# Kernel tuning notes

Hardware: AMD Instinct MI355X
Metric: run time of the kernel (lower is better)

Reference implementation:

```python
import jax, jax.numpy as jnp
import numpy as np

EMBED_DIM = 1024
NUM_HEADS = 16
HEAD_DIM = EMBED_DIM // NUM_HEADS


def setup_inputs() -> dict:
    key = jax.random.key(0)
    ks = jax.random.split(key, 5)
    x = jax.random.normal(ks[0], (2, 2048, EMBED_DIM), dtype=jnp.float32)
    s_in = 1.0 / np.sqrt(EMBED_DIM)
    W_qkv = jax.random.uniform(ks[1], (EMBED_DIM, 3 * EMBED_DIM), minval=-s_in, maxval=s_in, dtype=jnp.float32)
    b_qkv = jax.random.uniform(ks[2], (3 * EMBED_DIM,), minval=-s_in, maxval=s_in, dtype=jnp.float32)
    W_out = jax.random.uniform(ks[3], (EMBED_DIM, EMBED_DIM), minval=-s_in, maxval=s_in, dtype=jnp.float32)
    b_out = jax.random.uniform(ks[4], (EMBED_DIM,), minval=-s_in, maxval=s_in, dtype=jnp.float32)
    return {"x": x, "W_qkv": W_qkv, "b_qkv": b_qkv, "W_out": W_out, "b_out": b_out}


def reference(x, W_qkv, b_qkv, W_out, b_out):
    B, S, D = x.shape
    H, Dh = NUM_HEADS, HEAD_DIM
    qkv = x @ W_qkv + b_qkv                       # [B, S, 3D]
    q, k, v = jnp.split(qkv, 3, axis=-1)
    # [B, S, D] -> [B, H, S, Dh]
    q = q.reshape(B, S, H, Dh).transpose(0, 2, 1, 3)
    k = k.reshape(B, S, H, Dh).transpose(0, 2, 1, 3)
    v = v.reshape(B, S, H, Dh).transpose(0, 2, 1, 3)
    scores = jnp.einsum('bhqd,bhkd->bhqk', q, k) / jnp.sqrt(jnp.float32(Dh))
    probs = jax.nn.softmax(scores, axis=-1)       # [B, H, S, S]
    attn = jnp.einsum('bhqk,bhkd->bhqd', probs, v)
    attn = attn.transpose(0, 2, 1, 3).reshape(B, S, D)
    return attn @ W_out + b_out
```

## Files before the change

kernel.cpp:

```cpp
#include <hip/hip_runtime.h>
#include <hip/hip_bf16.h>

#define DEV __device__ __forceinline__

typedef __bf16 bf16x8 __attribute__((ext_vector_type(8)));
typedef float f32x4 __attribute__((ext_vector_type(4)));
typedef float f32x16 __attribute__((ext_vector_type(16)));
using u16 = unsigned short;
using u32 = unsigned int;

static constexpr int S = 2048;
static constexpr int D = 1024;
static constexpr float SCQ = 0.125f * 1.44269504088896340736f;

DEV u16 f2bf(float f) {
  unsigned u = __builtin_bit_cast(unsigned, f);
  u += 0x7fffu + ((u >> 16) & 1u);
  return (u16)(u >> 16);
}
DEV u16 f2bfr(float f) {
  return (u16)((__builtin_bit_cast(u32, f) + 0x8000u) >> 16);
}
DEV u32 pk2(float a, float b) {
  u32 ua = __builtin_bit_cast(u32, a) + 0x8000u;
  u32 ub = __builtin_bit_cast(u32, b) + 0x8000u;
  return __builtin_amdgcn_perm(ub, ua, 0x07060302);
}

DEV void gl16(const u16* __restrict__ g, u16* l) {
  __builtin_amdgcn_global_load_lds((const __attribute__((address_space(1))) u32*)g,
                                   (__attribute__((address_space(3))) u32*)l, 16, 0, 0);
}

__global__ __launch_bounds__(256) void k_prep(const float* __restrict__ x, u16* __restrict__ Xb,
                                              const float* __restrict__ Wqkv, u16* __restrict__ WqkvT,
                                              const float* __restrict__ Wout, u16* __restrict__ WoutT) {
  __shared__ float t[32][33];
  const int bid = blockIdx.x;
  const int tid = threadIdx.x;
  if (bid < 4096) {
    const int i = bid * 256 + tid;
    const float4 v = reinterpret_cast<const float4*>(x)[i];
    ushort4 o;
    o.x = f2bf(v.x); o.y = f2bf(v.y); o.z = f2bf(v.z); o.w = f2bf(v.w);
    reinterpret_cast<ushort4*>(Xb)[i] = o;
    return;
  }
  const float* in;
  u16* out;
  int R, C, bx, by;
  if (bid < 4096 + 3072) {
    const int b = bid - 4096;
    in = Wqkv; out = WqkvT; R = 1024; C = 3072;
    bx = b % 96; by = b / 96;
  } else {
    const int b = bid - 7168;
    in = Wout; out = WoutT; R = 1024; C = 1024;
    bx = b & 31; by = b >> 5;
  }
  const int tx = tid & 31, ty = tid >> 5;
  const int c0 = bx * 32, r0 = by * 32;
  for (int i = ty; i < 32; i += 8)
    t[i][tx] = in[(size_t)(r0 + i) * C + c0 + tx];
  __syncthreads();
  for (int i = ty; i < 32; i += 8)
    out[(size_t)(c0 + i) * R + r0 + tx] = f2bf(t[tx][i]);
}

template <int MODE, int TN>
__global__ __launch_bounds__(256) void k_gemm(const u16* __restrict__ A, const u16* __restrict__ Bt,
                                              const float* __restrict__ bias, int M, int N, int K,
                                              u16* __restrict__ Qb, u16* __restrict__ Kb,
                                              u16* __restrict__ Vt, float* __restrict__ outF) {
  constexpr int NJ = TN / 32;
  __shared__ u16 As[2][128][32];
  __shared__ u16 Bs[2][TN][32];
  const int tid = threadIdx.x;
  const int lane = tid & 63, wave = tid >> 6;
  const int l15 = lane & 15, quad = lane >> 4;
  const int m0 = blockIdx.y * 128, n0 = blockIdx.x * TN;
  const int wm = (wave >> 1) * 64, wn = (wave & 1) * (TN / 2);
  const int lr = lane >> 2;
  const int lcs = ((((lane & 3) - (lane >> 3)) & 3)) * 8;
  const int sq = ((quad + (l15 >> 1)) & 3) * 8;

  f32x4 acc[4][NJ];
#pragma unroll
  for (int i = 0; i < 4; i++)
#pragma unroll
    for (int j = 0; j < NJ; j++) acc[i][j] = (f32x4){0.f, 0.f, 0.f, 0.f};

  const u16* Aw0 = &A[(size_t)(m0 + wave * 32 + lr) * K + lcs];
  const u16* Aw1 = &A[(size_t)(m0 + wave * 32 + 16 + lr) * K + lcs];
  const u16* Bw0;
  const u16* Bw1;
  if constexpr (TN == 128) {
    Bw0 = &Bt[(size_t)(n0 + wave * 32 + lr) * K + lcs];
    Bw1 = &Bt[(size_t)(n0 + wave * 32 + 16 + lr) * K + lcs];
  } else {
    Bw0 = &Bt[(size_t)(n0 + wave * 16 + lr) * K + lcs];
  }

  gl16(Aw0, &As[0][wave * 32][0]);
  gl16(Aw1, &As[0][wave * 32 + 16][0]);
  if constexpr (TN == 128) {
    gl16(Bw0, &Bs[0][wave * 32][0]);
    gl16(Bw1, &Bs[0][wave * 32 + 16][0]);
  } else {
    gl16(Bw0, &Bs[0][wave * 16][0]);
  }

  int cur = 0;
#pragma unroll 2
  for (int kk = 0; kk < K; kk += 32, cur ^= 1) {
    __syncthreads();
    if (kk + 32 < K) {
      gl16(Aw0 + kk + 32, &As[cur ^ 1][wave * 32][0]);
      gl16(Aw1 + kk + 32, &As[cur ^ 1][wave * 32 + 16][0]);
      if constexpr (TN == 128) {
        gl16(Bw0 + kk + 32, &Bs[cur ^ 1][wave * 32][0]);
        gl16(Bw1 + kk + 32, &Bs[cur ^ 1][wave * 32 + 16][0]);
      } else {
        gl16(Bw0 + kk + 32, &Bs[cur ^ 1][wave * 16][0]);
      }
    }
    bf16x8 af[4], bfv[NJ];
#pragma unroll
    for (int i = 0; i < 4; i++)
      af[i] = *reinterpret_cast<const bf16x8*>(&As[cur][wm + i * 16 + l15][sq]);
#pragma unroll
    for (int j = 0; j < NJ; j++)
      bfv[j] = *reinterpret_cast<const bf16x8*>(&Bs[cur][wn + j * 16 + l15][sq]);
#pragma unroll
    for (int i = 0; i < 4; i++)
#pragma unroll
      for (int j = 0; j < NJ; j++)
        acc[i][j] = __builtin_amdgcn_mfma_f32_16x16x32_bf16(af[i], bfv[j], acc[i][j], 0, 0, 0);
  }

  if constexpr (MODE == 0) {
    __shared__ u16 LT[64][136];
    if (n0 >= 2048) {
      const int b = m0 >> 11, sbase = m0 & 2047;
#pragma unroll
      for (int p = 0; p < 2; p++) {
        __syncthreads();
        if ((wave & 1) == p) {
#pragma unroll
          for (int j = 0; j < NJ; j++) {
            const int n = n0 + wn + j * 16 + l15;
            const float vb = bias[n];
#pragma unroll
            for (int i = 0; i < 4; i++) {
              uint2 pw;
              pw.x = pk2(acc[i][j][0] + vb, acc[i][j][1] + vb);
              pw.y = pk2(acc[i][j][2] + vb, acc[i][j][3] + vb);
              *reinterpret_cast<uint2*>(&LT[j * 16 + l15][wm + i * 16 + quad * 4]) = pw;
            }
          }
        }
        __syncthreads();
        const int h = ((n0 - 2048) >> 6) + p;
        const int bh = b * 16 + h;
        const int nl = tid >> 2, cc = (tid & 3) * 32;
        u16* dst = &Vt[((size_t)bh * 64 + nl) * S + sbase + cc];
#pragma unroll
        for (int k = 0; k < 4; k++)
          reinterpret_cast<uint4*>(dst)[k] = *reinterpret_cast<const uint4*>(&LT[nl][cc + k * 8]);
      }
    } else {
#pragma unroll
      for (int i = 0; i < 4; i++) {
#pragma unroll
        for (int j = 0; j < NJ; j++) {
#pragma unroll
          for (int r = 0; r < 4; r++) {
            const int m = m0 + wm + i * 16 + quad * 4 + r;
            const int n = n0 + wn + j * 16 + l15;
            const float v = acc[i][j][r] + bias[n];
            const int h = (n >> 6) & 15, dh = n & 63;
            const int b = m >> 11, s = m & 2047;
            const int bh = b * 16 + h;
            if (n < 1024) Qb[((size_t)bh * S + s) * 64 + dh] = f2bfr(v * SCQ);
            else          Kb[((size_t)bh * S + s) * 64 + dh] = f2bfr(v);
          }
        }
      }
    }
  } else {
#pragma unroll
    for (int i = 0; i < 4; i++)
#pragma unroll
      for (int j = 0; j < NJ; j++)
#pragma unroll
        for (int r = 0; r < 4; r++) {
          const int m = m0 + wm + i * 16 + quad * 4 + r;
          const int n = n0 + wn + j * 16 + l15;
          outF[(size_t)m * N + n] = acc[i][j][r] + bias[n];
        }
  }
}

__global__ __launch_bounds__(256, 2) void k_attn(const u16* __restrict__ Qb,
                                                 const u16* __restrict__ Kb,
                                                 const u16* __restrict__ Vt,
                                                 u16* __restrict__ attnB) {
  __shared__ u16 Ks[64][72];
  __shared__ u16 Vs[64][72];
  __shared__ u16 Pl[4][32][72];
  const int bh = blockIdx.y;
  const int q0 = blockIdx.x * 128;
  const int tid = threadIdx.x;
  const int lane = tid & 63, wave = tid >> 6;
  const int l31 = lane & 31, hi = lane >> 5;
  const u16* Qh = Qb + (size_t)bh * S * 64;
  const u16* Kh = Kb + (size_t)bh * S * 64;
  const u16* Vh = Vt + (size_t)bh * 64 * S;
  const int qrow = q0 + wave * 32 + l31;
  bf16x8 qf[4];
#pragma unroll
  for (int f = 0; f < 4; f++)
    qf[f] = *reinterpret_cast<const bf16x8*>(&Qh[(size_t)qrow * 64 + f * 16 + hi * 8]);

  const int r0 = tid >> 3, c0 = (tid & 7) * 8;

  float li = 0.f;
  f32x16 o0, o1;
#pragma unroll
  for (int r = 0; r < 16; r++) { o0[r] = 0.f; o1[r] = 0.f; }

  uint4 pk0 = *reinterpret_cast<const uint4*>(&Kh[(size_t)r0 * 64 + c0]);
  uint4 pk1 = *reinterpret_cast<const uint4*>(&Kh[(size_t)(r0 + 32) * 64 + c0]);
  uint4 pv0 = *reinterpret_cast<const uint4*>(&Vh[(size_t)r0 * S + c0]);
  uint4 pv1 = *reinterpret_cast<const uint4*>(&Vh[(size_t)(r0 + 32) * S + c0]);

  for (int kb = 0; kb < S / 64; kb++) {
    __syncthreads();
    *reinterpret_cast<uint4*>(&Ks[r0][c0]) = pk0;
    *reinterpret_cast<uint4*>(&Ks[r0 + 32][c0]) = pk1;
    *reinterpret_cast<uint4*>(&Vs[r0][c0]) = pv0;
    *reinterpret_cast<uint4*>(&Vs[r0 + 32][c0]) = pv1;
    __syncthreads();
    if (kb + 1 < S / 64) {
      const u16* Kn = Kh + (size_t)(kb + 1) * 64 * 64;
      pk0 = *reinterpret_cast<const uint4*>(&Kn[(size_t)r0 * 64 + c0]);
      pk1 = *reinterpret_cast<const uint4*>(&Kn[(size_t)(r0 + 32) * 64 + c0]);
      pv0 = *reinterpret_cast<const uint4*>(&Vh[(size_t)r0 * S + (kb + 1) * 64 + c0]);
      pv1 = *reinterpret_cast<const uint4*>(&Vh[(size_t)(r0 + 32) * S + (kb + 1) * 64 + c0]);
    }
    f32x16 z[2];
#pragma unroll
    for (int kt = 0; kt < 2; kt++) {
#pragma unroll
      for (int r = 0; r < 16; r++) z[kt][r] = 0.f;
#pragma unroll
      for (int f = 0; f < 4; f++) {
        const bf16x8 a = *reinterpret_cast<const bf16x8*>(&Ks[kt * 32 + l31][f * 16 + hi * 8]);
        z[kt] = __builtin_amdgcn_mfma_f32_32x32x16_bf16(a, qf[f], z[kt], 0, 0, 0);
      }
    }
    float s0 = 0.f, s1 = 0.f, s2 = 0.f, s3 = 0.f;
#pragma unroll
    for (int kt = 0; kt < 2; kt++)
#pragma unroll
      for (int r = 0; r < 16; r++) {
        const float p = __builtin_amdgcn_exp2f(z[kt][r]);
        z[kt][r] = p;
        if ((r & 3) == 0) s0 += p; else if ((r & 3) == 1) s1 += p;
        else if ((r & 3) == 2) s2 += p; else s3 += p;
      }
    li += (s0 + s1) + (s2 + s3);
#pragma unroll
    for (int kt = 0; kt < 2; kt++)
#pragma unroll
      for (int g = 0; g < 4; g++) {
        uint2 pw;
        pw.x = pk2(z[kt][g * 4 + 0], z[kt][g * 4 + 1]);
        pw.y = pk2(z[kt][g * 4 + 2], z[kt][g * 4 + 3]);
        *reinterpret_cast<uint2*>(&Pl[wave][l31][kt * 32 + g * 8 + hi * 4]) = pw;
      }
#pragma unroll
    for (int f = 0; f < 4; f++) {
      const bf16x8 bp = *reinterpret_cast<const bf16x8*>(&Pl[wave][l31][f * 16 + hi * 8]);
      const bf16x8 av0 = *reinterpret_cast<const bf16x8*>(&Vs[l31][f * 16 + hi * 8]);
      const bf16x8 av1 = *reinterpret_cast<const bf16x8*>(&Vs[32 + l31][f * 16 + hi * 8]);
      o0 = __builtin_amdgcn_mfma_f32_32x32x16_bf16(av0, bp, o0, 0, 0, 0);
      o1 = __builtin_amdgcn_mfma_f32_32x32x16_bf16(av1, bp, o1, 0, 0, 0);
    }
  }
  li += __shfl_xor(li, 32);
  const float inv = 1.f / li;
#pragma unroll
  for (int dt = 0; dt < 2; dt++) {
    const f32x16& od = dt ? o1 : o0;
#pragma unroll
    for (int g = 0; g < 4; g++) {
      uint2 ow;
      ow.x = pk2(od[g * 4 + 0] * inv, od[g * 4 + 1] * inv);
      ow.y = pk2(od[g * 4 + 2] * inv, od[g * 4 + 3] * inv);
      *reinterpret_cast<uint2*>(&Pl[wave][l31][dt * 32 + g * 8 + hi * 4]) = ow;
    }
  }
  const int b = bh >> 4, h = bh & 15;
  const int mbase = b * S + q0 + wave * 32;
  const int qr = lane >> 1, ch = (lane & 1) * 32;
  u16* dst = &attnB[(size_t)(mbase + qr) * D + h * 64 + ch];
#pragma unroll
  for (int c = 0; c < 4; c++)
    reinterpret_cast<uint4*>(dst)[c] = *reinterpret_cast<const uint4*>(&Pl[wave][qr][ch + c * 8]);
}

extern "C" void kernel_launch(void* const* d_in, const int* in_sizes, int n_in,
                              void* d_out, int out_size, void* d_ws, size_t ws_size,
                              hipStream_t stream) {
  const float* x = (const float*)d_in[0];
  const float* Wqkv = (const float*)d_in[1];
  const float* bqkv = (const float*)d_in[2];
  const float* Wout = (const float*)d_in[3];
  const float* bout = (const float*)d_in[4];
  float* out = (float*)d_out;

  char* p = (char*)d_ws;
  u16* Xb = (u16*)p;    p += (size_t)4096 * 1024 * 2;
  u16* WqkvT = (u16*)p; p += (size_t)3072 * 1024 * 2;
  u16* WoutT = (u16*)p; p += (size_t)1024 * 1024 * 2;
  u16* Qb = (u16*)p;    p += (size_t)32 * 2048 * 64 * 2;
  u16* Kb = (u16*)p;    p += (size_t)32 * 2048 * 64 * 2;
  u16* Vt = (u16*)p;    p += (size_t)32 * 64 * 2048 * 2;
  u16* attnB = (u16*)p; p += (size_t)4096 * 1024 * 2;

  k_prep<<<4096 + 3072 + 1024, 256, 0, stream>>>(x, Xb, Wqkv, WqkvT, Wout, WoutT);
  k_gemm<0, 128><<<dim3(3072 / 128, 4096 / 128), 256, 0, stream>>>(
      Xb, WqkvT, bqkv, 4096, 3072, 1024, Qb, Kb, Vt, nullptr);
  k_attn<<<dim3(2048 / 128, 32), 256, 0, stream>>>(Qb, Kb, Vt, attnB);
  k_gemm<1, 64><<<dim3(1024 / 64, 4096 / 128), 256, 0, stream>>>(
      attnB, WoutT, bout, 4096, 1024, 1024, nullptr, nullptr, nullptr, out);
}
```

Before: 202.5 us.

## Split GEMM template; alias epilogue LDS and deepen K-tile for output projection

The templated GEMM becomes two specialized kernels. The QKV GEMM reuses the operand LDS buffers for the V-transpose staging tile and raises its occupancy hint to 5 blocks per CU. The output-projection GEMM uses a 64-wide K tile with an XOR-swizzled LDS layout, compile-time K/N and two MFMA k-steps per barrier. This halves the number of barrier iterations and reduces LDS footprint, at the cost of more registers and possible spills under the tighter launch bound.

```diff
diff --git a/kernel.cpp b/kernel.cpp
--- a/kernel.cpp
+++ b/kernel.cpp
@@ -67,14 +67,16 @@
     out[(size_t)(c0 + i) * R + r0 + tx] = f2bf(t[tx][i]);
 }
 
-template <int MODE, int TN>
-__global__ __launch_bounds__(256) void k_gemm(const u16* __restrict__ A, const u16* __restrict__ Bt,
-                                              const float* __restrict__ bias, int M, int N, int K,
-                                              u16* __restrict__ Qb, u16* __restrict__ Kb,
-                                              u16* __restrict__ Vt, float* __restrict__ outF) {
-  constexpr int NJ = TN / 32;
-  __shared__ u16 As[2][128][32];
-  __shared__ u16 Bs[2][TN][32];
+__global__ __launch_bounds__(256, 5) void k_gemm0(const u16* __restrict__ A, const u16* __restrict__ Bt,
+                                                  const float* __restrict__ bias, int M, int N, int K,
+                                                  u16* __restrict__ Qb, u16* __restrict__ Kb,
+                                                  u16* __restrict__ Vt) {
+  constexpr int TN = 128, NJ = 4;
+  constexpr int ASZ = 2 * 128 * 32 * 2;
+  __shared__ __align__(16) char smem[ASZ + 2 * TN * 32 * 2];
+  auto As = reinterpret_cast<u16(*)[128][32]>(smem);
+  auto Bs = reinterpret_cast<u16(*)[TN][32]>(smem + ASZ);
+  auto LT = reinterpret_cast<u16(*)[136]>(smem);
   const int tid = threadIdx.x;
   const int lane = tid & 63, wave = tid >> 6;
   const int l15 = lane & 15, quad = lane >> 4;
@@ -92,23 +94,13 @@
 
   const u16* Aw0 = &A[(size_t)(m0 + wave * 32 + lr) * K + lcs];
   const u16* Aw1 = &A[(size_t)(m0 + wave * 32 + 16 + lr) * K + lcs];
-  const u16* Bw0;
-  const u16* Bw1;
-  if constexpr (TN == 128) {
-    Bw0 = &Bt[(size_t)(n0 + wave * 32 + lr) * K + lcs];
-    Bw1 = &Bt[(size_t)(n0 + wave * 32 + 16 + lr) * K + lcs];
-  } else {
-    Bw0 = &Bt[(size_t)(n0 + wave * 16 + lr) * K + lcs];
-  }
+  const u16* Bw0 = &Bt[(size_t)(n0 + wave * 32 + lr) * K + lcs];
+  const u16* Bw1 = &Bt[(size_t)(n0 + wave * 32 + 16 + lr) * K + lcs];
 
   gl16(Aw0, &As[0][wave * 32][0]);
   gl16(Aw1, &As[0][wave * 32 + 16][0]);
-  if constexpr (TN == 128) {
-    gl16(Bw0, &Bs[0][wave * 32][0]);
-    gl16(Bw1, &Bs[0][wave * 32 + 16][0]);
-  } else {
-    gl16(Bw0, &Bs[0][wave * 16][0]);
-  }
+  gl16(Bw0, &Bs[0][wave * 32][0]);
+  gl16(Bw1, &Bs[0][wave * 32 + 16][0]);
 
   int cur = 0;
 #pragma unroll 2
@@ -117,12 +109,8 @@
     if (kk + 32 < K) {
       gl16(Aw0 + kk + 32, &As[cur ^ 1][wave * 32][0]);
       gl16(Aw1 + kk + 32, &As[cur ^ 1][wave * 32 + 16][0]);
-      if constexpr (TN == 128) {
-        gl16(Bw0 + kk + 32, &Bs[cur ^ 1][wave * 32][0]);
-        gl16(Bw1 + kk + 32, &Bs[cur ^ 1][wave * 32 + 16][0]);
-      } else {
-        gl16(Bw0 + kk + 32, &Bs[cur ^ 1][wave * 16][0]);
-      }
+      gl16(Bw0 + kk + 32, &Bs[cur ^ 1][wave * 32][0]);
+      gl16(Bw1 + kk + 32, &Bs[cur ^ 1][wave * 32 + 16][0]);
     }
     bf16x8 af[4], bfv[NJ];
 #pragma unroll
@@ -138,67 +126,128 @@
         acc[i][j] = __builtin_amdgcn_mfma_f32_16x16x32_bf16(af[i], bfv[j], acc[i][j], 0, 0, 0);
   }
 
-  if constexpr (MODE == 0) {
-    __shared__ u16 LT[64][136];
-    if (n0 >= 2048) {
-      const int b = m0 >> 11, sbase = m0 & 2047;
-#pragma unroll
-      for (int p = 0; p < 2; p++) {
-        __syncthreads();
-        if ((wave & 1) == p) {
-#pragma unroll
-          for (int j = 0; j < NJ; j++) {
-            const int n = n0 + wn + j * 16 + l15;
-            const float vb = bias[n];
-#pragma unroll
-            for (int i = 0; i < 4; i++) {
-              uint2 pw;
-              pw.x = pk2(acc[i][j][0] + vb, acc[i][j][1] + vb);
-              pw.y = pk2(acc[i][j][2] + vb, acc[i][j][3] + vb);
-              *reinterpret_cast<uint2*>(&LT[j * 16 + l15][wm + i * 16 + quad * 4]) = pw;
-            }
+  if (n0 >= 2048) {
+    const int b = m0 >> 11, sbase = m0 & 2047;
+#pragma unroll
+    for (int p = 0; p < 2; p++) {
+      __syncthreads();
+      if ((wave & 1) == p) {
+#pragma unroll
+        for (int j = 0; j < NJ; j++) {
+          const int n = n0 + wn + j * 16 + l15;
+          const float vb = bias[n];
+#pragma unroll
+          for (int i = 0; i < 4; i++) {
+            uint2 pw;
+            pw.x = pk2(acc[i][j][0] + vb, acc[i][j][1] + vb);
+            pw.y = pk2(acc[i][j][2] + vb, acc[i][j][3] + vb);
+            *reinterpret_cast<uint2*>(&LT[j * 16 + l15][wm + i * 16 + quad * 4]) = pw;
           }
         }
-        __syncthreads();
-        const int h = ((n0 - 2048) >> 6) + p;
-        const int bh = b * 16 + h;
-        const int nl = tid >> 2, cc = (tid & 3) * 32;
-        u16* dst = &Vt[((size_t)bh * 64 + nl) * S + sbase + cc];
-#pragma unroll
-        for (int k = 0; k < 4; k++)
-          reinterpret_cast<uint4*>(dst)[k] = *reinterpret_cast<const uint4*>(&LT[nl][cc + k * 8]);
-      }
-    } else {
-#pragma unroll
-      for (int i = 0; i < 4; i++) {
-#pragma unroll
-        for (int j = 0; j < NJ; j++) {
-#pragma unroll
-          for (int r = 0; r < 4; r++) {
-            const int m = m0 + wm + i * 16 + quad * 4 + r;
-            const int n = n0 + wn + j * 16 + l15;
-            const float v = acc[i][j][r] + bias[n];
-            const int h = (n >> 6) & 15, dh = n & 63;
-            const int b = m >> 11, s = m & 2047;
-            const int bh = b * 16 + h;
-            if (n < 1024) Qb[((size_t)bh * S + s) * 64 + dh] = f2bfr(v * SCQ);
-            else          Kb[((size_t)bh * S + s) * 64 + dh] = f2bfr(v);
-          }
-        }
-      }
+      }
+      __syncthreads();
+      const int h = ((n0 - 2048) >> 6) + p;
+      const int bh = b * 16 + h;
+      const int nl = tid >> 2, cc = (tid & 3) * 32;
+      u16* dst = &Vt[((size_t)bh * 64 + nl) * S + sbase + cc];
+#pragma unroll
+      for (int k = 0; k < 4; k++)
+        reinterpret_cast<uint4*>(dst)[k] = *reinterpret_cast<const uint4*>(&LT[nl][cc + k * 8]);
     }
   } else {
 #pragma unroll
-    for (int i = 0; i < 4; i++)
-#pragma unroll
-      for (int j = 0; j < NJ; j++)
+    for (int i = 0; i < 4; i++) {
+#pragma unroll
+      for (int j = 0; j < NJ; j++) {
 #pragma unroll
         for (int r = 0; r < 4; r++) {
           const int m = m0 + wm + i * 16 + quad * 4 + r;
           const int n = n0 + wn + j * 16 + l15;
-          outF[(size_t)m * N + n] = acc[i][j][r] + bias[n];
+          const float v = acc[i][j][r] + bias[n];
+          const int h = (n >> 6) & 15, dh = n & 63;
+          const int b = m >> 11, s = m & 2047;
+          const int bh = b * 16 + h;
+          if (n < 1024) Qb[((size_t)bh * S + s) * 64 + dh] = f2bfr(v * SCQ);
+          else          Kb[((size_t)bh * S + s) * 64 + dh] = f2bfr(v);
         }
-  }
+      }
+    }
+  }
+}
+
+__global__ __launch_bounds__(256, 2) void k_gemm2(const u16* __restrict__ A, const u16* __restrict__ Bt,
+                                                  const float* __restrict__ bias, float* __restrict__ outF) {
+  constexpr int K = 1024, N = 1024;
+  constexpr int ASZ = 2 * 128 * 64 * 2;
+  __shared__ __align__(16) char smem[ASZ + 2 * 64 * 64 * 2];
+  auto As = reinterpret_cast<u16(*)[128][64]>(smem);
+  auto Bs = reinterpret_cast<u16(*)[64][64]>(smem + ASZ);
+  const int tid = threadIdx.x;
+  const int lane = tid & 63, wave = tid >> 6;
+  const int l15 = lane & 15, quad = lane >> 4;
+  const int m0 = blockIdx.y * 128, n0 = blockIdx.x * 64;
+  const int wm = (wave >> 1) * 64, wn = (wave & 1) * 32;
+  const int srow = lane >> 3;
+  const int scol = ((lane & 7) ^ (lane >> 3)) * 8;
+
+  f32x4 acc[4][2];
+#pragma unroll
+  for (int i = 0; i < 4; i++)
+#pragma unroll
+    for (int j = 0; j < 2; j++) acc[i][j] = (f32x4){0.f, 0.f, 0.f, 0.f};
+
+  const u16* Ap[4];
+  const u16* Bp[2];
+#pragma unroll
+  for (int c = 0; c < 4; c++)
+    Ap[c] = &A[(size_t)(m0 + (wave * 4 + c) * 8 + srow) * K + scol];
+#pragma unroll
+  for (int c = 0; c < 2; c++)
+    Bp[c] = &Bt[(size_t)(n0 + (wave * 2 + c) * 8 + srow) * K + scol];
+
+#pragma unroll
+  for (int c = 0; c < 4; c++) gl16(Ap[c], &As[0][(wave * 4 + c) * 8][0]);
+#pragma unroll
+  for (int c = 0; c < 2; c++) gl16(Bp[c], &Bs[0][(wave * 2 + c) * 8][0]);
+
+  int cur = 0;
+#pragma unroll 2
+  for (int kk = 0; kk < K; kk += 64, cur ^= 1) {
+    __syncthreads();
+    if (kk + 64 < K) {
+#pragma unroll
+      for (int c = 0; c < 4; c++) gl16(Ap[c] + kk + 64, &As[cur ^ 1][(wave * 4 + c) * 8][0]);
+#pragma unroll
+      for (int c = 0; c < 2; c++) gl16(Bp[c] + kk + 64, &Bs[cur ^ 1][(wave * 2 + c) * 8][0]);
+    }
+#pragma unroll
+    for (int ks = 0; ks < 2; ks++) {
+      const int sc = ((ks * 4 + quad) ^ (l15 & 7)) * 8;
+      bf16x8 af[4], bfv[2];
+#pragma unroll
+      for (int i = 0; i < 4; i++)
+        af[i] = *reinterpret_cast<const bf16x8*>(&As[cur][wm + i * 16 + l15][sc]);
+#pragma unroll
+      for (int j = 0; j < 2; j++)
+        bfv[j] = *reinterpret_cast<const bf16x8*>(&Bs[cur][wn + j * 16 + l15][sc]);
+#pragma unroll
+      for (int i = 0; i < 4; i++)
+#pragma unroll
+        for (int j = 0; j < 2; j++)
+          acc[i][j] = __builtin_amdgcn_mfma_f32_16x16x32_bf16(af[i], bfv[j], acc[i][j], 0, 0, 0);
+    }
+  }
+
+#pragma unroll
+  for (int i = 0; i < 4; i++)
+#pragma unroll
+    for (int j = 0; j < 2; j++)
+#pragma unroll
+      for (int r = 0; r < 4; r++) {
+        const int m = m0 + wm + i * 16 + quad * 4 + r;
+        const int n = n0 + wn + j * 16 + l15;
+        outF[(size_t)m * N + n] = acc[i][j][r] + bias[n];
+      }
 }
 
 __global__ __launch_bounds__(256, 2) void k_attn(const u16* __restrict__ Qb,
@@ -330,9 +379,8 @@
   u16* attnB = (u16*)p; p += (size_t)4096 * 1024 * 2;
 
   k_prep<<<4096 + 3072 + 1024, 256, 0, stream>>>(x, Xb, Wqkv, WqkvT, Wout, WoutT);
-  k_gemm<0, 128><<<dim3(3072 / 128, 4096 / 128), 256, 0, stream>>>(
-      Xb, WqkvT, bqkv, 4096, 3072, 1024, Qb, Kb, Vt, nullptr);
+  k_gemm0<<<dim3(3072 / 128, 4096 / 128), 256, 0, stream>>>(
+      Xb, WqkvT, bqkv, 4096, 3072, 1024, Qb, Kb, Vt);
   k_attn<<<dim3(2048 / 128, 32), 256, 0, stream>>>(Qb, Kb, Vt, attnB);
-  k_gemm<1, 64><<<dim3(1024 / 64, 4096 / 128), 256, 0, stream>>>(
-      attnB, WoutT, bout, 4096, 1024, 1024, nullptr, nullptr, nullptr, out);
-}
+  k_gemm2<<<dim3(1024 / 64, 4096 / 128), 256, 0, stream>>>(attnB, WoutT, bout, out);
+}
```

Result: faster. 190.5 us (-5.9%).
